# Kernel tuning notes

Hardware: AMD Instinct MI355X
Metric: run time of the kernel (lower is better)

The kernel has to match this reference:

```python
import jax, jax.numpy as jnp
import numpy as np

DOWNSAMPLE = 4
REG = 0.05
SINKHORN_ITERS = 50
LAMBDA_OT = 1.0
LAMBDA_TV = 1.0


def setup_inputs() -> dict:
    key = jax.random.key(0)
    k1, k2 = jax.random.split(key)
    pred = jax.random.uniform(k1, (16, 1, 256, 256), dtype=jnp.float32)
    gt = jax.random.uniform(k2, (16, 1, 256, 256), dtype=jnp.float32)
    return {"pred": pred, "gt": gt, "epoch": 5, "max_epoch": 10}


def _avg_pool(x, k):
    B, C, H, W = x.shape
    return x.reshape(B, C, H // k, k, W // k, k).mean(axis=(3, 5))


def _normalize(x, n):
    # relu then normalize to a distribution; fall back to uniform if sum==0
    x = jnp.maximum(x, 0.0)
    s = x.sum(axis=1, keepdims=True)  # [B,1]
    return jnp.where(s > 0, x / s, jnp.full_like(x, 1.0 / n))


def _curriculum_loss(pred, gt, epoch, max_epoch):
    B = pred.shape[0]
    # --- counting loss: L1 between total counts ---
    pc = pred.reshape(B, -1).sum(axis=1)
    gc = gt.reshape(B, -1).sum(axis=1)
    l_count = jnp.abs(pc - gc).mean()

    t = float(epoch) / float(max(1, max_epoch))
    ot_w = LAMBDA_OT * t
    tv_w = LAMBDA_TV * t

    # --- OT loss (batched Sinkhorn) ---
    pd = _avg_pool(pred, DOWNSAMPLE)
    gd = _avg_pool(gt, DOWNSAMPLE)
    h, w = pd.shape[2], pd.shape[3]
    n = h * w
    ys = jnp.arange(h, dtype=jnp.float32)
    xs = jnp.arange(w, dtype=jnp.float32)
    yy, xx = jnp.meshgrid(ys, xs, indexing="ij")
    yf = yy.reshape(-1)  # [n]
    xf = xx.reshape(-1)
    # squared euclidean cost matrix [n,n], built separably (no [n,n,2] temp)
    M = (yf[:, None] - yf[None, :]) ** 2 + (xf[:, None] - xf[None, :]) ** 2
    K = jnp.exp(-M / REG)  # [n,n]

    a = _normalize(pd.reshape(B, -1), n)  # [B,n]
    b = _normalize(gd.reshape(B, -1), n)

    def step(uv, _):
        u, v = uv
        u = a / (v @ K.T)  # K @ v per sample, batched
        v = b / (u @ K)    # K.T @ u per sample, batched
        return (u, v), None

    ones = jnp.ones((B, n), dtype=pred.dtype)
    (u, v), _ = jax.lax.scan(step, (ones, ones), None, length=SINKHORN_ITERS)
    # cost_b = sum_ij u_i K_ij v_j M_ij
    cost = jnp.einsum("bn,nm,bm->b", u, K * M, v)
    l_ot = cost.mean()

    # --- total variation loss ---
    dx = jnp.abs(pred[:, :, :, 1:] - pred[:, :, :, :-1]).mean()
    dy = jnp.abs(pred[:, :, 1:, :] - pred[:, :, :-1, :]).mean()
    l_tv = dx + dy

    return l_count + ot_w * l_ot + tv_w * l_tv


def reference(pred, gt, epoch, max_epoch):
    return _curriculum_loss(pred, gt, epoch, max_epoch)
```

## Files before the change

### kernel.cpp

```cpp
#include <hip/hip_runtime.h>
#include <math.h>


#define KW1 2.0611536224385578e-09f
#define MW2 8.4967085105831778e-18f
#define RP2 72

__device__ __forceinline__ float dpp_left(float x) {
  return __int_as_float(__builtin_amdgcn_update_dpp(
      0, __float_as_int(x), 0x111, 0xF, 0xF, true));
}
__device__ __forceinline__ float dpp_right(float x) {
  return __int_as_float(__builtin_amdgcn_update_dpp(
      0, __float_as_int(x), 0x101, 0xF, 0xF, true));
}

__device__ __forceinline__ float ad4(const float4 a, const float4 b) {
  return fabsf(a.x - b.x) + fabsf(a.y - b.y) + fabsf(a.z - b.z) + fabsf(a.w - b.w);
}

__device__ __forceinline__ void hrow4(const float f[4], float h[4]) {
  const float l = dpp_left(f[3]);
  const float r = dpp_right(f[0]);
  h[0] = fmaf(KW1, l + f[1], f[0]);
  h[1] = fmaf(KW1, f[0] + f[2], f[1]);
  h[2] = fmaf(KW1, f[1] + f[3], f[2]);
  h[3] = fmaf(KW1, f[2] + r, f[3]);
}

__device__ __forceinline__ void phase_core(
    const float prev[4][4], float ph[4][4],
    const float cf0[4], const float cf3[4],
    float2 mA, float4 mB, float2 mC, float2 pA, float4 pB, float2 pC,
    float* __restrict__ RT_wr, float* __restrict__ RB_wr, int wb,
    float out0[4], float out3[4]) {
  hrow4(prev[0], ph[0]); hrow4(prev[1], ph[1]);
  hrow4(prev[2], ph[2]); hrow4(prev[3], ph[3]);
  float hm[4], hp[4];
  hm[0] = fmaf(KW1, mA.y + mB.y, mB.x);
  hm[1] = fmaf(KW1, mB.x + mB.z, mB.y);
  hm[2] = fmaf(KW1, mB.y + mB.w, mB.z);
  hm[3] = fmaf(KW1, mB.z + mC.x, mB.w);
  hp[0] = fmaf(KW1, pA.y + pB.y, pB.x);
  hp[1] = fmaf(KW1, pB.x + pB.z, pB.y);
  hp[2] = fmaf(KW1, pB.y + pB.w, pB.z);
  hp[3] = fmaf(KW1, pB.z + pC.x, pB.w);
#pragma unroll
  for (int j = 0; j < 4; ++j)
    out0[j] = cf0[j] * __builtin_amdgcn_rcpf(fmaf(KW1, hm[j] + ph[1][j], ph[0][j]));
#pragma unroll
  for (int j = 0; j < 4; ++j)
    out3[j] = cf3[j] * __builtin_amdgcn_rcpf(fmaf(KW1, ph[2][j] + hp[j], ph[3][j]));
  *(float4*)&RT_wr[wb] = make_float4(out0[0], out0[1], out0[2], out0[3]);
  *(float4*)&RB_wr[wb] = make_float4(out3[0], out3[1], out3[2], out3[3]);
}

__global__ __launch_bounds__(256) void fused_kernel(
    const float* __restrict__ pred, const float* __restrict__ gt,
    float* __restrict__ ws, const int* __restrict__ epoch,
    const int* __restrict__ max_epoch, float* __restrict__ out,
    unsigned int* __restrict__ cnt) {
  __shared__ float RTu[18 * RP2], RBu[18 * RP2];
  __shared__ float RTv[18 * RP2], RBv[18 * RP2];
  __shared__ float rbuf[24];

  const int b = blockIdx.x;
  const int t = threadIdx.x;
  const int tyg = t >> 4, tx = t & 15;
  const int y0 = tyg * 4, x0 = tx * 4;

  for (int i = t; i < 18 * RP2; i += 256) {
    RTu[i] = 0.f; RBu[i] = 0.f; RTv[i] = 0.f; RBv[i] = 0.f;
  }

  const float* pb = pred + b * 65536;
  const float* gb = gt + b * 65536;
  const int sr0 = 4 * y0, sc0 = 4 * x0;

  float pd[4][4], gd[4][4];
  float4 pr0, pr1, pr2, pr3;
  float spraw = 0.f, sgraw = 0.f, sx = 0.f, sy = 0.f;
#pragma unroll
  for (int i = 0; i < 4; ++i) {
    float a0 = 0.f, a1 = 0.f, a2 = 0.f, a3 = 0.f;
    float c0 = 0.f, c1 = 0.f, c2 = 0.f, c3 = 0.f;
#pragma unroll 1
    for (int rr = 0; rr < 4; ++rr) {
      const int r = i * 4 + rr;
      const float* prow = pb + (sr0 + r) * 256 + sc0;
      const float4 q0 = *(const float4*)(prow);
      const float4 q1 = *(const float4*)(prow + 4);
      const float4 q2 = *(const float4*)(prow + 8);
      const float4 q3 = *(const float4*)(prow + 12);
      const float s0 = (q0.x + q0.y) + (q0.z + q0.w);
      const float s1 = (q1.x + q1.y) + (q1.z + q1.w);
      const float s2 = (q2.x + q2.y) + (q2.z + q2.w);
      const float s3 = (q3.x + q3.y) + (q3.z + q3.w);
      a0 += s0; a1 += s1; a2 += s2; a3 += s3;
      spraw += (s0 + s1) + (s2 + s3);
      sx += fabsf(q0.y - q0.x) + fabsf(q0.z - q0.y) + fabsf(q0.w - q0.z)
          + fabsf(q1.x - q0.w)
          + fabsf(q1.y - q1.x) + fabsf(q1.z - q1.y) + fabsf(q1.w - q1.z)
          + fabsf(q2.x - q1.w)
          + fabsf(q2.y - q2.x) + fabsf(q2.z - q2.y) + fabsf(q2.w - q2.z)
          + fabsf(q3.x - q2.w)
          + fabsf(q3.y - q3.x) + fabsf(q3.z - q3.y) + fabsf(q3.w - q3.z);
      const float nf = dpp_right(q0.x);
      if (tx < 15) sx += fabsf(nf - q3.w);
      if (r > 0) sy += ad4(q0, pr0) + ad4(q1, pr1) + ad4(q2, pr2) + ad4(q3, pr3);
      pr0 = q0; pr1 = q1; pr2 = q2; pr3 = q3;
      const float* grow = gb + (sr0 + r) * 256 + sc0;
      const float4 g0 = *(const float4*)(grow);
      const float4 g1 = *(const float4*)(grow + 4);
      const float4 g2 = *(const float4*)(grow + 8);
      const float4 g3 = *(const float4*)(grow + 12);
      const float u0 = (g0.x + g0.y) + (g0.z + g0.w);
      const float u1 = (g1.x + g1.y) + (g1.z + g1.w);
      const float u2 = (g2.x + g2.y) + (g2.z + g2.w);
      const float u3 = (g3.x + g3.y) + (g3.z + g3.w);
      c0 += u0; c1 += u1; c2 += u2; c3 += u3;
      sgraw += (u0 + u1) + (u2 + u3);
    }
    pd[i][0] = a0; pd[i][1] = a1; pd[i][2] = a2; pd[i][3] = a3;
    gd[i][0] = c0; gd[i][1] = c1; gd[i][2] = c2; gd[i][3] = c3;
  }
  if (tyg < 15) {
    const float* prow = pb + (sr0 + 16) * 256 + sc0;
    sy += ad4(*(const float4*)(prow), pr0) + ad4(*(const float4*)(prow + 4), pr1)
        + ad4(*(const float4*)(prow + 8), pr2) + ad4(*(const float4*)(prow + 12), pr3);
  }

  float spd = 0.f, sgd = 0.f;
#pragma unroll
  for (int i = 0; i < 4; ++i)
#pragma unroll
    for (int j = 0; j < 4; ++j) {
      pd[i][j] = fmaxf(pd[i][j] * 0.0625f, 0.f); spd += pd[i][j];
      gd[i][j] = fmaxf(gd[i][j] * 0.0625f, 0.f); sgd += gd[i][j];
    }

  float r0 = spraw, r1 = sgraw, r2 = spd, r3 = sgd, r4 = sx, r5 = sy;
#pragma unroll
  for (int o = 32; o > 0; o >>= 1) {
    r0 += __shfl_down(r0, o); r1 += __shfl_down(r1, o);
    r2 += __shfl_down(r2, o); r3 += __shfl_down(r3, o);
    r4 += __shfl_down(r4, o); r5 += __shfl_down(r5, o);
  }
  if ((t & 63) == 0) {
    const int w = t >> 6;
    rbuf[w * 6 + 0] = r0; rbuf[w * 6 + 1] = r1; rbuf[w * 6 + 2] = r2;
    rbuf[w * 6 + 3] = r3; rbuf[w * 6 + 4] = r4; rbuf[w * 6 + 5] = r5;
  }
  __syncthreads();
  if (t == 0) {
    float a0 = 0, a1 = 0, a2 = 0, a3 = 0, a4 = 0, a5 = 0;
    for (int w = 0; w < 4; ++w) {
      a0 += rbuf[w * 6 + 0]; a1 += rbuf[w * 6 + 1]; a2 += rbuf[w * 6 + 2];
      a3 += rbuf[w * 6 + 3]; a4 += rbuf[w * 6 + 4]; a5 += rbuf[w * 6 + 5];
    }
    ws[b] = a0; ws[16 + b] = a1; ws[48 + b] = a4; ws[64 + b] = a5;
    rbuf[0] = a2; rbuf[1] = a3;
  }
  __syncthreads();
  const float Sp = rbuf[0], Sg = rbuf[1];

  float av[4][4], bv[4][4];
#pragma unroll
  for (int i = 0; i < 4; ++i)
#pragma unroll
    for (int j = 0; j < 4; ++j) {
      av[i][j] = (Sp > 0.f) ? (pd[i][j] / Sp) : (1.f / 4096.f);
      bv[i][j] = (Sg > 0.f) ? (gd[i][j] / Sg) : (1.f / 4096.f);
    }

  const int rbb = tyg * RP2 + x0 + 2;
  const int rtb = (tyg + 2) * RP2 + x0 + 2;
  const int wb  = (1 + tyg) * RP2 + 4 + x0;

  float uu[4][4], vv[4][4], uh[4][4], vh[4][4];
#pragma unroll
  for (int i = 0; i < 4; ++i)
#pragma unroll
    for (int j = 0; j < 4; ++j) vv[i][j] = 1.f;
  *(float4*)&RTv[wb] = make_float4(1.f, 1.f, 1.f, 1.f);
  *(float4*)&RBv[wb] = make_float4(1.f, 1.f, 1.f, 1.f);
  __syncthreads();

#pragma unroll 1
  for (int it = 0; it < 50; ++it) {
    {
      const float2 mA = *(const float2*)&RBv[rbb];
      const float4 mB = *(const float4*)&RBv[rbb + 2];
      const float2 mC = *(const float2*)&RBv[rbb + 6];
      const float2 pA = *(const float2*)&RTv[rtb];
      const float4 pB = *(const float4*)&RTv[rtb + 2];
      const float2 pC = *(const float2*)&RTv[rtb + 6];
      if (it != 0) {
#pragma unroll
        for (int j = 0; j < 4; ++j) {
          vv[1][j] = bv[1][j] * __builtin_amdgcn_rcpf(fmaf(KW1, uh[0][j] + uh[2][j], uh[1][j]));
          vv[2][j] = bv[2][j] * __builtin_amdgcn_rcpf(fmaf(KW1, uh[1][j] + uh[3][j], uh[2][j]));
        }
      }
      phase_core(vv, vh, av[0], av[3], mA, mB, mC, pA, pB, pC,
                 RTu, RBu, wb, uu[0], uu[3]);
    }
    __syncthreads();
    {
      const float2 mA = *(const float2*)&RBu[rbb];
      const float4 mB = *(const float4*)&RBu[rbb + 2];
      const float2 mC = *(const float2*)&RBu[rbb + 6];
      const float2 pA = *(const float2*)&RTu[rtb];
      const float4 pB = *(const float4*)&RTu[rtb + 2];
      const float2 pC = *(const float2*)&RTu[rtb + 6];
#pragma unroll
      for (int j = 0; j < 4; ++j) {
        uu[1][j] = av[1][j] * __builtin_amdgcn_rcpf(fmaf(KW1, vh[0][j] + vh[2][j], vh[1][j]));
        uu[2][j] = av[2][j] * __builtin_amdgcn_rcpf(fmaf(KW1, vh[1][j] + vh[3][j], vh[2][j]));
      }
      phase_core(uu, uh, bv[0], bv[3], mA, mB, mC, pA, pB, pC,
                 RTv, RBv, wb, vv[0], vv[3]);
    }
    __syncthreads();
  }

#pragma unroll
  for (int j = 0; j < 4; ++j) {
    vv[1][j] = bv[1][j] * __builtin_amdgcn_rcpf(fmaf(KW1, uh[0][j] + uh[2][j], uh[1][j]));
    vv[2][j] = bv[2][j] * __builtin_amdgcn_rcpf(fmaf(KW1, uh[1][j] + uh[3][j], uh[2][j]));
  }

  float c = 0.f;
  {
    const float2 mA = *(const float2*)&RBv[rbb];
    const float4 mB = *(const float4*)&RBv[rbb + 2];
    const float2 mC = *(const float2*)&RBv[rbb + 6];
    const float2 pA = *(const float2*)&RTv[rtb];
    const float4 pB = *(const float4*)&RTv[rtb + 2];
    const float2 pC = *(const float2*)&RTv[rtb + 6];
    float W[6][6];
    W[0][0] = mA.y; W[0][1] = mB.x; W[0][2] = mB.y;
    W[0][3] = mB.z; W[0][4] = mB.w; W[0][5] = mC.x;
    W[5][0] = pA.y; W[5][1] = pB.x; W[5][2] = pB.y;
    W[5][3] = pB.z; W[5][4] = pB.w; W[5][5] = pC.x;
#pragma unroll
    for (int i = 0; i < 4; ++i) {
      W[1 + i][0] = dpp_left(vv[i][3]);
      W[1 + i][5] = dpp_right(vv[i][0]);
#pragma unroll
      for (int j = 0; j < 4; ++j) W[1 + i][1 + j] = vv[i][j];
    }
#pragma unroll
    for (int i = 0; i < 4; ++i)
#pragma unroll
      for (int j = 0; j < 4; ++j) {
        const float e = (W[i][j + 1] + W[i + 2][j + 1])
                      + (W[i + 1][j] + W[i + 1][j + 2]);
        const float d = (W[i][j] + W[i][j + 2])
                      + (W[i + 2][j] + W[i + 2][j + 2]);
        c += uu[i][j] * fmaf(MW2, d, KW1 * e);
      }
  }
#pragma unroll
  for (int o = 32; o > 0; o >>= 1) c += __shfl_down(c, o);
  if ((t & 63) == 0) rbuf[t >> 6] = c;
  __syncthreads();
  if (t == 0) {
    ws[32 + b] = rbuf[0] + rbuf[1] + rbuf[2] + rbuf[3];
    __threadfence();
    const unsigned int old = atomicAdd(cnt, 1u);
    if (old == 15u) {
      __threadfence();
      float lc = 0.f, lot = 0.f, tvx = 0.f, tvy = 0.f;
      for (int k = 0; k < 16; ++k) {
        const float p  = __hip_atomic_load(&ws[k],      __ATOMIC_RELAXED, __HIP_MEMORY_SCOPE_AGENT);
        const float g  = __hip_atomic_load(&ws[16 + k], __ATOMIC_RELAXED, __HIP_MEMORY_SCOPE_AGENT);
        const float ct = __hip_atomic_load(&ws[32 + k], __ATOMIC_RELAXED, __HIP_MEMORY_SCOPE_AGENT);
        const float x  = __hip_atomic_load(&ws[48 + k], __ATOMIC_RELAXED, __HIP_MEMORY_SCOPE_AGENT);
        const float y  = __hip_atomic_load(&ws[64 + k], __ATOMIC_RELAXED, __HIP_MEMORY_SCOPE_AGENT);
        lc += fabsf(p - g); lot += ct; tvx += x; tvy += y;
      }
      int me = max_epoch[0]; if (me < 1) me = 1;
      const float tt = (float)epoch[0] / (float)me;
      const float ltv = tvx / (16.f * 256.f * 255.f) + tvy / (16.f * 255.f * 256.f);
      out[0] = lc * (1.f / 16.f) + tt * (lot * (1.f / 16.f)) + tt * ltv;
    }
  }
}

extern "C" void kernel_launch(void* const* d_in, const int* in_sizes, int n_in,
                              void* d_out, int out_size, void* d_ws, size_t ws_size,
                              hipStream_t stream) {
  const float* pred = (const float*)d_in[0];
  const float* gt   = (const float*)d_in[1];
  const int* epoch  = (const int*)d_in[2];
  const int* max_ep = (const int*)d_in[3];
  float* out = (float*)d_out;
  float* ws  = (float*)d_ws;
  unsigned int* cnt = (unsigned int*)((char*)d_ws + 384);

  hipMemsetAsync(cnt, 0, 4, stream);
  fused_kernel<<<dim3(16), dim3(256), 0, stream>>>(pred, gt, ws, epoch,
                                                   max_ep, out, cnt);
}
```

Before: 120.8 us.

## Split pooling/TV/count reduction into wide prep kernel before Sinkhorn kernel

Moves the full-resolution reads (4x4 average pooling, count sums and total-variation sums) into a separate 256-block prep kernel that writes the pooled maps and partial sums to the workspace. A second 16-block kernel then runs the Sinkhorn iterations from the pooled data and does the final reduction in parallel across threads. This spreads the memory-bound part over many CUs instead of only 16 blocks, at the cost of an extra launch and a workspace round trip. The old fused path is kept as a fallback when the workspace is too small.

```diff
diff --git a/kernel.cpp b/kernel.cpp
--- a/kernel.cpp
+++ b/kernel.cpp
@@ -5,6 +5,8 @@
 #define KW1 2.0611536224385578e-09f
 #define MW2 8.4967085105831778e-18f
 #define RP2 72
+#define PDOFF 2048
+#define GDOFF 67584
 
 __device__ __forceinline__ float dpp_left(float x) {
   return __int_as_float(__builtin_amdgcn_update_dpp(
@@ -17,6 +19,10 @@
 
 __device__ __forceinline__ float ad4(const float4 a, const float4 b) {
   return fabsf(a.x - b.x) + fabsf(a.y - b.y) + fabsf(a.z - b.z) + fabsf(a.w - b.w);
+}
+
+__device__ __forceinline__ float agent_ld(const float* p) {
+  return __hip_atomic_load(p, __ATOMIC_RELAXED, __HIP_MEMORY_SCOPE_AGENT);
 }
 
 __device__ __forceinline__ void hrow4(const float f[4], float h[4]) {
@@ -55,7 +61,250 @@
   *(float4*)&RB_wr[wb] = make_float4(out3[0], out3[1], out3[2], out3[3]);
 }
 
-__global__ __launch_bounds__(256) void fused_kernel(
+__global__ __launch_bounds__(256) void prep_kernel(
+    const float* __restrict__ pred, const float* __restrict__ gt,
+    float* __restrict__ ws) {
+  __shared__ float rbuf[16];
+  const int g = blockIdx.x;
+  const int im = g >> 4, band = g & 15;
+  const int t = threadIdx.x;
+  const int ppy = t >> 6, ppx = t & 63;
+  const float* pb = pred + im * 65536;
+  const float* gb = gt + im * 65536;
+  const int sr0 = band * 16 + ppy * 4;
+  const int c0 = ppx * 4;
+
+  float4 q[4];
+  float ps = 0.f, gs = 0.f, sx = 0.f, sy = 0.f;
+#pragma unroll
+  for (int r = 0; r < 4; ++r) {
+    q[r] = *(const float4*)(pb + (sr0 + r) * 256 + c0);
+    const float4 e = *(const float4*)(gb + (sr0 + r) * 256 + c0);
+    ps += (q[r].x + q[r].y) + (q[r].z + q[r].w);
+    gs += (e.x + e.y) + (e.z + e.w);
+    sx += fabsf(q[r].y - q[r].x) + fabsf(q[r].z - q[r].y) + fabsf(q[r].w - q[r].z);
+    const float nf = __shfl_down(q[r].x, 1);
+    if (ppx < 63) sx += fabsf(nf - q[r].w);
+  }
+  sy += ad4(q[1], q[0]) + ad4(q[2], q[1]) + ad4(q[3], q[2]);
+  if (sr0 + 4 < 256) {
+    const float4 qn = *(const float4*)(pb + (sr0 + 4) * 256 + c0);
+    sy += ad4(qn, q[3]);
+  }
+  const int prow = band * 4 + ppy;
+  ws[PDOFF + im * 4096 + prow * 64 + ppx] = fmaxf(ps * 0.0625f, 0.f);
+  ws[GDOFF + im * 4096 + prow * 64 + ppx] = fmaxf(gs * 0.0625f, 0.f);
+
+  float r0 = ps, r1 = gs, r2 = sx, r3 = sy;
+#pragma unroll
+  for (int o = 32; o > 0; o >>= 1) {
+    r0 += __shfl_down(r0, o); r1 += __shfl_down(r1, o);
+    r2 += __shfl_down(r2, o); r3 += __shfl_down(r3, o);
+  }
+  if ((t & 63) == 0) {
+    const int w = t >> 6;
+    rbuf[w * 4 + 0] = r0; rbuf[w * 4 + 1] = r1;
+    rbuf[w * 4 + 2] = r2; rbuf[w * 4 + 3] = r3;
+  }
+  __syncthreads();
+  if (t == 0) {
+    float a0 = 0, a1 = 0, a2 = 0, a3 = 0;
+    for (int w = 0; w < 4; ++w) {
+      a0 += rbuf[w * 4]; a1 += rbuf[w * 4 + 1];
+      a2 += rbuf[w * 4 + 2]; a3 += rbuf[w * 4 + 3];
+    }
+    ws[g] = a0; ws[256 + g] = a1; ws[512 + g] = a2; ws[768 + g] = a3;
+  }
+}
+
+__global__ __launch_bounds__(256) void sink_kernel(
+    float* __restrict__ ws, const int* __restrict__ epoch,
+    const int* __restrict__ max_epoch, float* __restrict__ out,
+    unsigned int* __restrict__ cnt) {
+  __shared__ float RTu[18 * RP2], RBu[18 * RP2];
+  __shared__ float RTv[18 * RP2], RBv[18 * RP2];
+  __shared__ float rbuf[24];
+  __shared__ int lastflag;
+
+  const int b = blockIdx.x;
+  const int t = threadIdx.x;
+  const int tyg = t >> 4, tx = t & 15;
+  const int y0 = tyg * 4, x0 = tx * 4;
+
+  for (int i = t; i < 18 * RP2; i += 256) {
+    RTu[i] = 0.f; RBu[i] = 0.f; RTv[i] = 0.f; RBv[i] = 0.f;
+  }
+
+  float pdv[4][4], gdv[4][4];
+  float spd = 0.f, sgd = 0.f;
+#pragma unroll
+  for (int i = 0; i < 4; ++i) {
+    const float4 qa = *(const float4*)&ws[PDOFF + b * 4096 + (y0 + i) * 64 + x0];
+    pdv[i][0] = qa.x; pdv[i][1] = qa.y; pdv[i][2] = qa.z; pdv[i][3] = qa.w;
+    spd += (qa.x + qa.y) + (qa.z + qa.w);
+    const float4 qb = *(const float4*)&ws[GDOFF + b * 4096 + (y0 + i) * 64 + x0];
+    gdv[i][0] = qb.x; gdv[i][1] = qb.y; gdv[i][2] = qb.z; gdv[i][3] = qb.w;
+    sgd += (qb.x + qb.y) + (qb.z + qb.w);
+  }
+  float r2 = spd, r3 = sgd;
+#pragma unroll
+  for (int o = 32; o > 0; o >>= 1) { r2 += __shfl_down(r2, o); r3 += __shfl_down(r3, o); }
+  if ((t & 63) == 0) { rbuf[(t >> 6) * 2] = r2; rbuf[(t >> 6) * 2 + 1] = r3; }
+  __syncthreads();
+  if (t == 0) {
+    rbuf[16] = rbuf[0] + rbuf[2] + rbuf[4] + rbuf[6];
+    rbuf[17] = rbuf[1] + rbuf[3] + rbuf[5] + rbuf[7];
+  }
+  __syncthreads();
+  const float Sp = rbuf[16], Sg = rbuf[17];
+
+  float av[4][4], bv[4][4];
+#pragma unroll
+  for (int i = 0; i < 4; ++i)
+#pragma unroll
+    for (int j = 0; j < 4; ++j) {
+      av[i][j] = (Sp > 0.f) ? (pdv[i][j] / Sp) : (1.f / 4096.f);
+      bv[i][j] = (Sg > 0.f) ? (gdv[i][j] / Sg) : (1.f / 4096.f);
+    }
+
+  const int rbb = tyg * RP2 + x0 + 2;
+  const int rtb = (tyg + 2) * RP2 + x0 + 2;
+  const int wb  = (1 + tyg) * RP2 + 4 + x0;
+
+  float uu[4][4], vv[4][4], uh[4][4], vh[4][4];
+#pragma unroll
+  for (int i = 0; i < 4; ++i)
+#pragma unroll
+    for (int j = 0; j < 4; ++j) vv[i][j] = 1.f;
+  *(float4*)&RTv[wb] = make_float4(1.f, 1.f, 1.f, 1.f);
+  *(float4*)&RBv[wb] = make_float4(1.f, 1.f, 1.f, 1.f);
+  __syncthreads();
+
+#pragma unroll 1
+  for (int it = 0; it < 50; ++it) {
+    {
+      const float2 mA = *(const float2*)&RBv[rbb];
+      const float4 mB = *(const float4*)&RBv[rbb + 2];
+      const float2 mC = *(const float2*)&RBv[rbb + 6];
+      const float2 pA = *(const float2*)&RTv[rtb];
+      const float4 pB = *(const float4*)&RTv[rtb + 2];
+      const float2 pC = *(const float2*)&RTv[rtb + 6];
+      if (it != 0) {
+#pragma unroll
+        for (int j = 0; j < 4; ++j) {
+          vv[1][j] = bv[1][j] * __builtin_amdgcn_rcpf(fmaf(KW1, uh[0][j] + uh[2][j], uh[1][j]));
+          vv[2][j] = bv[2][j] * __builtin_amdgcn_rcpf(fmaf(KW1, uh[1][j] + uh[3][j], uh[2][j]));
+        }
+      }
+      phase_core(vv, vh, av[0], av[3], mA, mB, mC, pA, pB, pC,
+                 RTu, RBu, wb, uu[0], uu[3]);
+    }
+    __syncthreads();
+    {
+      const float2 mA = *(const float2*)&RBu[rbb];
+      const float4 mB = *(const float4*)&RBu[rbb + 2];
+      const float2 mC = *(const float2*)&RBu[rbb + 6];
+      const float2 pA = *(const float2*)&RTu[rtb];
+      const float4 pB = *(const float4*)&RTu[rtb + 2];
+      const float2 pC = *(const float2*)&RTu[rtb + 6];
+#pragma unroll
+      for (int j = 0; j < 4; ++j) {
+        uu[1][j] = av[1][j] * __builtin_amdgcn_rcpf(fmaf(KW1, vh[0][j] + vh[2][j], vh[1][j]));
+        uu[2][j] = av[2][j] * __builtin_amdgcn_rcpf(fmaf(KW1, vh[1][j] + vh[3][j], vh[2][j]));
+      }
+      phase_core(uu, uh, bv[0], bv[3], mA, mB, mC, pA, pB, pC,
+                 RTv, RBv, wb, vv[0], vv[3]);
+    }
+    __syncthreads();
+  }
+#pragma unroll
+  for (int j = 0; j < 4; ++j) {
+    vv[1][j] = bv[1][j] * __builtin_amdgcn_rcpf(fmaf(KW1, uh[0][j] + uh[2][j], uh[1][j]));
+    vv[2][j] = bv[2][j] * __builtin_amdgcn_rcpf(fmaf(KW1, uh[1][j] + uh[3][j], uh[2][j]));
+  }
+
+  float c = 0.f;
+  {
+    const float2 mA = *(const float2*)&RBv[rbb];
+    const float4 mB = *(const float4*)&RBv[rbb + 2];
+    const float2 mC = *(const float2*)&RBv[rbb + 6];
+    const float2 pA = *(const float2*)&RTv[rtb];
+    const float4 pB = *(const float4*)&RTv[rtb + 2];
+    const float2 pC = *(const float2*)&RTv[rtb + 6];
+    float W[6][6];
+    W[0][0] = mA.y; W[0][1] = mB.x; W[0][2] = mB.y;
+    W[0][3] = mB.z; W[0][4] = mB.w; W[0][5] = mC.x;
+    W[5][0] = pA.y; W[5][1] = pB.x; W[5][2] = pB.y;
+    W[5][3] = pB.z; W[5][4] = pB.w; W[5][5] = pC.x;
+#pragma unroll
+    for (int i = 0; i < 4; ++i) {
+      W[1 + i][0] = dpp_left(vv[i][3]);
+      W[1 + i][5] = dpp_right(vv[i][0]);
+#pragma unroll
+      for (int j = 0; j < 4; ++j) W[1 + i][1 + j] = vv[i][j];
+    }
+#pragma unroll
+    for (int i = 0; i < 4; ++i)
+#pragma unroll
+      for (int j = 0; j < 4; ++j) {
+        const float e = (W[i][j + 1] + W[i + 2][j + 1])
+                      + (W[i + 1][j] + W[i + 1][j + 2]);
+        const float d = (W[i][j] + W[i][j + 2])
+                      + (W[i + 2][j] + W[i + 2][j + 2]);
+        c += uu[i][j] * fmaf(MW2, d, KW1 * e);
+      }
+  }
+#pragma unroll
+  for (int o = 32; o > 0; o >>= 1) c += __shfl_down(c, o);
+  if ((t & 63) == 0) rbuf[t >> 6] = c;
+  __syncthreads();
+  if (t == 0) {
+    ws[1024 + b] = rbuf[0] + rbuf[1] + rbuf[2] + rbuf[3];
+    __threadfence();
+    const unsigned int old = atomicAdd(cnt, 1u);
+    lastflag = (old == 15u) ? 1 : 0;
+  }
+  __syncthreads();
+
+  if (lastflag) {
+    __threadfence();
+    float myPc = agent_ld(&ws[t]);
+    float myGc = agent_ld(&ws[256 + t]);
+    float myTx = agent_ld(&ws[512 + t]);
+    float myTy = agent_ld(&ws[768 + t]);
+#pragma unroll
+    for (int o = 8; o > 0; o >>= 1) {
+      myPc += __shfl_down(myPc, o, 16);
+      myGc += __shfl_down(myGc, o, 16);
+    }
+    float d = ((t & 15) == 0) ? fabsf(myPc - myGc) : 0.f;
+    float ct = (t < 16) ? agent_ld(&ws[1024 + t]) : 0.f;
+#pragma unroll
+    for (int o = 32; o > 0; o >>= 1) {
+      d += __shfl_down(d, o); ct += __shfl_down(ct, o);
+      myTx += __shfl_down(myTx, o); myTy += __shfl_down(myTy, o);
+    }
+    if ((t & 63) == 0) {
+      const int w = t >> 6;
+      rbuf[w * 4] = d; rbuf[w * 4 + 1] = ct;
+      rbuf[w * 4 + 2] = myTx; rbuf[w * 4 + 3] = myTy;
+    }
+    __syncthreads();
+    if (t == 0) {
+      float lc = 0, lot = 0, tvx = 0, tvy = 0;
+      for (int w = 0; w < 4; ++w) {
+        lc += rbuf[w * 4]; lot += rbuf[w * 4 + 1];
+        tvx += rbuf[w * 4 + 2]; tvy += rbuf[w * 4 + 3];
+      }
+      int me = max_epoch[0]; if (me < 1) me = 1;
+      const float tt = (float)epoch[0] / (float)me;
+      const float ltv = tvx / (16.f * 256.f * 255.f) + tvy / (16.f * 255.f * 256.f);
+      out[0] = lc * (1.f / 16.f) + tt * (lot * (1.f / 16.f)) + tt * ltv;
+    }
+  }
+}
+
+__global__ __launch_bounds__(256) void fused_fallback(
     const float* __restrict__ pred, const float* __restrict__ gt,
     float* __restrict__ ws, const int* __restrict__ epoch,
     const int* __restrict__ max_epoch, float* __restrict__ out,
@@ -223,7 +472,6 @@
     }
     __syncthreads();
   }
-
 #pragma unroll
   for (int j = 0; j < 4; ++j) {
     vv[1][j] = bv[1][j] * __builtin_amdgcn_rcpf(fmaf(KW1, uh[0][j] + uh[2][j], uh[1][j]));
@@ -273,11 +521,11 @@
       __threadfence();
       float lc = 0.f, lot = 0.f, tvx = 0.f, tvy = 0.f;
       for (int k = 0; k < 16; ++k) {
-        const float p  = __hip_atomic_load(&ws[k],      __ATOMIC_RELAXED, __HIP_MEMORY_SCOPE_AGENT);
-        const float g  = __hip_atomic_load(&ws[16 + k], __ATOMIC_RELAXED, __HIP_MEMORY_SCOPE_AGENT);
-        const float ct = __hip_atomic_load(&ws[32 + k], __ATOMIC_RELAXED, __HIP_MEMORY_SCOPE_AGENT);
-        const float x  = __hip_atomic_load(&ws[48 + k], __ATOMIC_RELAXED, __HIP_MEMORY_SCOPE_AGENT);
-        const float y  = __hip_atomic_load(&ws[64 + k], __ATOMIC_RELAXED, __HIP_MEMORY_SCOPE_AGENT);
+        const float p = agent_ld(&ws[k]);
+        const float g = agent_ld(&ws[16 + k]);
+        const float ct = agent_ld(&ws[32 + k]);
+        const float x = agent_ld(&ws[48 + k]);
+        const float y = agent_ld(&ws[64 + k]);
         lc += fabsf(p - g); lot += ct; tvx += x; tvy += y;
       }
       int me = max_epoch[0]; if (me < 1) me = 1;
@@ -297,9 +545,16 @@
   const int* max_ep = (const int*)d_in[3];
   float* out = (float*)d_out;
   float* ws  = (float*)d_ws;
-  unsigned int* cnt = (unsigned int*)((char*)d_ws + 384);
-
-  hipMemsetAsync(cnt, 0, 4, stream);
-  fused_kernel<<<dim3(16), dim3(256), 0, stream>>>(pred, gt, ws, epoch,
-                                                   max_ep, out, cnt);
-}
+
+  if (ws_size >= 600000) {
+    unsigned int* cnt = (unsigned int*)((char*)d_ws + 4160);
+    hipMemsetAsync(cnt, 0, 4, stream);
+    prep_kernel<<<dim3(256), dim3(256), 0, stream>>>(pred, gt, ws);
+    sink_kernel<<<dim3(16), dim3(256), 0, stream>>>(ws, epoch, max_ep, out, cnt);
+  } else {
+    unsigned int* cnt = (unsigned int*)((char*)d_ws + 384);
+    hipMemsetAsync(cnt, 0, 4, stream);
+    fused_fallback<<<dim3(16), dim3(256), 0, stream>>>(pred, gt, ws, epoch,
+                                                       max_ep, out, cnt);
+  }
+}
```

After: 111.5 us. -7.7%, faster.
